# Performance work log

Hardware: AMD Instinct MI355X
Metric: run time of the kernel (lower is better)

The kernel has to match this reference:

```python
import jax, jax.numpy as jnp
import numpy as np

# dims: T tokens, HID hidden, H heads, D head_dim, K conv kernel size
T, HID, H, D, K = 4096, 2048, 16, 128, 4
HD = H * D
EPS = 1e-6


def causal_conv(x, w):
    # depthwise causal conv: x [T, C], w [C, K]; y_t = sum_i w[:, i] * x_{t-K+1+i}
    xp = jnp.pad(x, ((K - 1, 0), (0, 0)))
    y = jnp.zeros_like(x)
    for i in range(K):  # small fixed kernel loop
        y = y + w[:, i] * xp[i:i + x.shape[0]]
    return y


def l2norm(x):
    return x * jax.lax.rsqrt(jnp.sum(x * x, -1, keepdims=True) + EPS)


def setup_inputs() -> dict:
    key = jax.random.key(0)
    ks = jax.random.split(key, 16)
    s = lambda n: 1.0 / np.sqrt(n)
    return {
        "hidden_states": jax.random.normal(ks[0], (T, HID), jnp.float32),
        "Wq": jax.random.normal(ks[1], (HID, HD), jnp.float32) * s(HID),
        "Wk": jax.random.normal(ks[2], (HID, HD), jnp.float32) * s(HID),
        "Wv": jax.random.normal(ks[3], (HID, HD), jnp.float32) * s(HID),
        "wq_conv": jax.random.normal(ks[4], (HD, K), jnp.float32) * s(K),
        "wk_conv": jax.random.normal(ks[5], (HD, K), jnp.float32) * s(K),
        "wv_conv": jax.random.normal(ks[6], (HD, K), jnp.float32) * s(K),
        "A_log": jax.random.uniform(ks[7], (H,), jnp.float32, 0.0, 0.5),
        "dt_bias": jax.random.normal(ks[8], (HD,), jnp.float32) * 0.1,
        "Wfa": jax.random.normal(ks[9], (HID, D), jnp.float32) * s(HID),
        "Wfb": jax.random.normal(ks[10], (D, HD), jnp.float32) * s(D),
        "Wb": jax.random.normal(ks[11], (HID, H), jnp.float32) * s(HID),
        "Wga": jax.random.normal(ks[12], (HID, D), jnp.float32) * s(HID),
        "Wgb": jax.random.normal(ks[13], (D, HD), jnp.float32) * s(D),
        "norm_w": jnp.ones((D,), jnp.float32),
        "Wo": jax.random.normal(ks[14], (HD, HID), jnp.float32) * s(HD),
    }


def reference(hidden_states, Wq, Wk, Wv, wq_conv, wk_conv, wv_conv, A_log,
              dt_bias, Wfa, Wfb, Wb, Wga, Wgb, norm_w, Wo):
    x = hidden_states
    # projections + short causal conv + SiLU
    q = jax.nn.silu(causal_conv(x @ Wq, wq_conv)).reshape(T, H, D)
    k = jax.nn.silu(causal_conv(x @ Wk, wk_conv)).reshape(T, H, D)
    v = jax.nn.silu(causal_conv(x @ Wv, wv_conv)).reshape(T, H, D)
    # fine-grained per-channel log-decay: g = -exp(A_log) * softplus(f + dt_bias), [T,H,D]
    f = (x @ Wfa) @ Wfb + dt_bias
    g = -(jnp.exp(A_log)[None, :, None]) * jax.nn.softplus(f.reshape(T, H, D))
    beta = jax.nn.sigmoid(x @ Wb)  # [T, H]
    q = l2norm(q)
    k = l2norm(k)
    scale = D ** -0.5

    def step(S, inp):  # S: [H, Dk, Dv]
        q_t, k_t, v_t, g_t, b_t = inp
        S = S * jnp.exp(g_t)[..., None]  # diagonal per-key-channel decay
        err = v_t - jnp.einsum('hkv,hk->hv', S, k_t)  # delta-rule error
        dv = b_t[:, None] * err  # beta gate
        S = S + k_t[:, :, None] * dv[:, None, :]
        o_t = jnp.einsum('hkv,hk->hv', S, q_t) * scale
        return S, o_t

    S0 = jnp.zeros((H, D, D), jnp.float32)
    _, o = jax.lax.scan(step, S0, (q, k, v, g, beta))  # o: [T, H, D]

    # gated RMSNorm then output projection
    gate = ((x @ Wga) @ Wgb).reshape(T, H, D)
    o = o * jax.lax.rsqrt(jnp.mean(o * o, -1, keepdims=True) + EPS)
    o = o * norm_w * jax.nn.silu(gate)
    return o.reshape(T, HD) @ Wo
```

## Files before the change

### kernel.cpp

```cpp
#include <hip/hip_runtime.h>
#include <hip/hip_bf16.h>
#include <math.h>

typedef __bf16 bf16_t;
typedef __bf16 bf16x8 __attribute__((ext_vector_type(8)));
typedef float  floatx4 __attribute__((ext_vector_type(4)));
typedef float  floatx2 __attribute__((ext_vector_type(2)));
typedef unsigned uintx4 __attribute__((ext_vector_type(4)));

constexpr int T_TOK = 4096;
constexpr int HID   = 2048;
constexpr int NH    = 16;
constexpr int DH    = 128;
constexpr int CH    = 2048;
constexpr int CHUNK = 16;
constexpr int NCH   = T_TOK / CHUNK;

__global__ __launch_bounds__(256) void cast_to_bf16(const float* __restrict__ in,
                                                    bf16_t* __restrict__ out, int n) {
  int i = (blockIdx.x * 256 + threadIdx.x) * 8;
  if (i >= n) return;
  float4 a = *(const float4*)(in + i);
  float4 b = *(const float4*)(in + i + 4);
  bf16x8 o;
  o[0]=(bf16_t)a.x; o[1]=(bf16_t)a.y; o[2]=(bf16_t)a.z; o[3]=(bf16_t)a.w;
  o[4]=(bf16_t)b.x; o[5]=(bf16_t)b.y; o[6]=(bf16_t)b.z; o[7]=(bf16_t)b.w;
  *(bf16x8*)(out + i) = o;
}

__global__ __launch_bounds__(256) void transpose_cast(const float* __restrict__ in,
                                                      bf16_t* __restrict__ out, int R, int C) {
  __shared__ float tile[32][33];
  int tx = threadIdx.x & 31;
  int ty = threadIdx.x >> 5;
  int r0 = blockIdx.x * 32;
  int c0 = blockIdx.y * 32;
#pragma unroll
  for (int i = 0; i < 4; i++) {
    int r = ty + i * 8;
    float v = 0.f;
    if (r0 + r < R && c0 + tx < C) v = in[(size_t)(r0 + r) * C + (c0 + tx)];
    tile[r][tx] = v;
  }
  __syncthreads();
#pragma unroll
  for (int i = 0; i < 4; i++) {
    int cr = ty + i * 8;
    if (c0 + cr < C && r0 + tx < R)
      out[(size_t)(c0 + cr) * R + (r0 + tx)] = (bf16_t)tile[tx][cr];
  }
}

template<bool OUT_BF16>
__global__ __launch_bounds__(256) void gemm_bf16(
    const bf16_t* __restrict__ A, int lda,
    const bf16_t* __restrict__ Bt, int ldb,
    void* __restrict__ Cv, int ldc, int M, int N, int K) {
  __shared__ bf16_t sA[128][40];
  __shared__ bf16_t sB[128][40];
  const int tid  = threadIdx.x;
  const int bm0  = blockIdx.x * 128;
  const int bn0  = blockIdx.y * 128;
  const int wave = tid >> 6;
  const int lane = tid & 63;
  const int wm   = (wave & 1) * 64;
  const int wn   = (wave >> 1) * 64;
  const int fm   = lane & 15;
  const int kq   = lane >> 4;

  floatx4 acc[4][4];
#pragma unroll
  for (int mi = 0; mi < 4; mi++)
#pragma unroll
    for (int ni = 0; ni < 4; ni++)
      acc[mi][ni] = (floatx4){0.f, 0.f, 0.f, 0.f};

  const int sr = tid >> 2;
  const int sk = (tid & 3) * 8;
  const bool bval0 = (bn0 + sr) < N;
  const bool bval1 = (bn0 + sr + 64) < N;
  const bf16_t* Ag0 = A + (size_t)(bm0 + sr) * lda + sk;
  const bf16_t* Ag1 = Ag0 + (size_t)64 * lda;
  const bf16_t* Bg0 = Bt + (size_t)(bn0 + sr) * ldb + sk;
  const bf16_t* Bg1 = Bg0 + (size_t)64 * ldb;

  for (int k0 = 0; k0 < K; k0 += 32) {
    float4 a0 = *(const float4*)(Ag0 + k0);
    float4 a1 = *(const float4*)(Ag1 + k0);
    float4 b0 = bval0 ? *(const float4*)(Bg0 + k0) : make_float4(0.f, 0.f, 0.f, 0.f);
    float4 b1 = bval1 ? *(const float4*)(Bg1 + k0) : make_float4(0.f, 0.f, 0.f, 0.f);
    __syncthreads();
    *(float4*)(&sA[sr][sk])      = a0;
    *(float4*)(&sA[sr + 64][sk]) = a1;
    *(float4*)(&sB[sr][sk])      = b0;
    *(float4*)(&sB[sr + 64][sk]) = b1;
    __syncthreads();
    bf16x8 afr[4], bfr[4];
#pragma unroll
    for (int i = 0; i < 4; i++) {
      afr[i] = *(const bf16x8*)(&sA[wm + i * 16 + fm][kq * 8]);
      bfr[i] = *(const bf16x8*)(&sB[wn + i * 16 + fm][kq * 8]);
    }
#pragma unroll
    for (int mi = 0; mi < 4; mi++)
#pragma unroll
      for (int ni = 0; ni < 4; ni++)
        acc[mi][ni] = __builtin_amdgcn_mfma_f32_16x16x32_bf16(afr[mi], bfr[ni], acc[mi][ni], 0, 0, 0);
  }

  const int rr = (lane >> 4) * 4;
#pragma unroll
  for (int mi = 0; mi < 4; mi++) {
#pragma unroll
    for (int r = 0; r < 4; r++) {
      const int row = bm0 + wm + mi * 16 + rr + r;
#pragma unroll
      for (int ni = 0; ni < 4; ni++) {
        const int col = bn0 + wn + ni * 16 + fm;
        if (col < N) {
          if constexpr (OUT_BF16)
            ((bf16_t*)Cv)[(size_t)row * ldc + col] = (bf16_t)acc[mi][ni][r];
          else
            ((float*)Cv)[(size_t)row * ldc + col] = acc[mi][ni][r];
        }
      }
    }
  }
}

template<bool L2NORM>
__global__ __launch_bounds__(256) void conv_silu(
    const bf16_t* __restrict__ raw, const float* __restrict__ wconv,
    bf16_t* __restrict__ out) {
  const int t   = blockIdx.x;
  const int tid = threadIdx.x;
  const int c0  = tid * 8;

  float w[8][4];
#pragma unroll
  for (int j = 0; j < 8; j++) {
    float4 t0 = *(const float4*)(wconv + (size_t)(c0 + j) * 4);
    w[j][0] = t0.x; w[j][1] = t0.y; w[j][2] = t0.z; w[j][3] = t0.w;
  }
  float a[8] = {};
#pragma unroll
  for (int i = 0; i < 4; i++) {
    int tr = t - 3 + i;
    if (tr < 0) continue;
    bf16x8 xr = *(const bf16x8*)(raw + (size_t)tr * CH + c0);
#pragma unroll
    for (int j = 0; j < 8; j++) a[j] += w[j][i] * (float)xr[j];
  }
  float s = 0.f;
#pragma unroll
  for (int j = 0; j < 8; j++) {
    a[j] = a[j] / (1.f + expf(-a[j]));
    s += a[j] * a[j];
  }
  float rs = 1.f;
  if constexpr (L2NORM) {
#pragma unroll
    for (int m = 1; m < 16; m <<= 1) s += __shfl_xor(s, m);
    rs = rsqrtf(s + 1e-6f);
  }
  bf16x8 r;
#pragma unroll
  for (int j = 0; j < 8; j++) r[j] = (bf16_t)(a[j] * rs);
  *(bf16x8*)(out + (size_t)t * CH + c0) = r;
}

__global__ __launch_bounds__(256) void gamma_beta(
    float* __restrict__ f_gam, const float* __restrict__ dt_bias,
    const float* __restrict__ A_log, float* __restrict__ beta_io) {
  const int t   = blockIdx.x;
  const int tid = threadIdx.x;
  const int c0  = tid * 8;
  const int h   = c0 >> 7;
  const float a_h = expf(A_log[h]);
  const size_t o0 = (size_t)t * CH + c0;
  float fv[8], db[8];
  { float4 f0 = *(const float4*)(f_gam + o0);   float4 f1 = *(const float4*)(f_gam + o0 + 4);
    fv[0]=f0.x; fv[1]=f0.y; fv[2]=f0.z; fv[3]=f0.w; fv[4]=f1.x; fv[5]=f1.y; fv[6]=f1.z; fv[7]=f1.w;
    float4 d0 = *(const float4*)(dt_bias + c0); float4 d1 = *(const float4*)(dt_bias + c0 + 4);
    db[0]=d0.x; db[1]=d0.y; db[2]=d0.z; db[3]=d0.w; db[4]=d1.x; db[5]=d1.y; db[6]=d1.z; db[7]=d1.w; }
  float og[8];
#pragma unroll
  for (int j = 0; j < 8; j++) {
    float f = fv[j] + db[j];
    float sp = (f > 20.f) ? f : log1pf(expf(f));
    og[j] = -a_h * sp;
  }
  *(float4*)(f_gam + o0)     = make_float4(og[0], og[1], og[2], og[3]);
  *(float4*)(f_gam + o0 + 4) = make_float4(og[4], og[5], og[6], og[7]);
  if (tid < NH) {
    float b = beta_io[(size_t)t * NH + tid];
    beta_io[(size_t)t * NH + tid] = 1.f / (1.f + expf(-b));
  }
}

template<int IMM>
__device__ __forceinline__ float swzf(float x) {
  return __builtin_bit_cast(float, __builtin_amdgcn_ds_swizzle(__builtin_bit_cast(int, x), IMM));
}
template<int CTRL>
__device__ __forceinline__ float dppadd(float x) {
  int v = __builtin_amdgcn_update_dpp(0, __builtin_bit_cast(int, x), CTRL, 0xF, 0xF, true);
  return x + __builtin_bit_cast(float, v);
}
__device__ __forceinline__ float cumsum16(float x) {
  x = dppadd<0x111>(x);
  x = dppadd<0x112>(x);
  x = dppadd<0x114>(x);
  x = dppadd<0x118>(x);
  return x;
}
__device__ __forceinline__ float bperm(int lane, float x) {
  return __builtin_bit_cast(float, __builtin_amdgcn_ds_bpermute(lane << 2, __builtin_bit_cast(int, x)));
}
__device__ __forceinline__ floatx2 bfpair(unsigned u) {
  floatx2 r;
  r[0] = __builtin_bit_cast(float, u << 16);
  r[1] = __builtin_bit_cast(float, u & 0xFFFF0000u);
  return r;
}

__global__ __launch_bounds__(64) void wy_prep(
    bf16_t* __restrict__ qn, bf16_t* __restrict__ kn,
    const float* __restrict__ gg, const float* __restrict__ beta,
    bf16_t* __restrict__ ktilT, float* __restrict__ Tm,
    bf16_t* __restrict__ MBf, float* __restrict__ ecT, float* __restrict__ e2T) {
  const int hc = blockIdx.x;
  const int h  = hc >> 8;
  const int c  = hc & 255;
  const int l  = threadIdx.x;
  const int tl = l & 15;
  const int gr = l >> 4;

  __shared__ bf16_t KldsT[128][24];
  __shared__ float  Wlds[16][17];
  __shared__ float  Mlds[16][17];
  __shared__ float  eclds[128], e2lds[128];
  __shared__ float  blds[16];

  const int kb0 = h * DH + gr * 8;
  const size_t rowoff = (size_t)(c * CHUNK + tl) * CH;

  if (gr == 0) blds[tl] = beta[(size_t)(c * CHUNK + tl) * NH + h];

  floatx4 wt = (floatx4){0.f, 0.f, 0.f, 0.f};
  floatx4 m  = (floatx4){0.f, 0.f, 0.f, 0.f};
  bf16x8 khs[4], qhs[4];
#pragma unroll
  for (int kb = 0; kb < 4; kb++) {
    const int ke = kb0 + kb * 32;
    float4 ga = *(const float4*)(gg + rowoff + ke);
    float4 gb = *(const float4*)(gg + rowoff + ke + 4);
    float cm[8] = {ga.x, ga.y, ga.z, ga.w, gb.x, gb.y, gb.z, gb.w};
    float lamh[8], lamt[8], ec[8], e2[8];
#pragma unroll
    for (int j = 0; j < 8; j++) {
      float cs   = cumsum16(cm[j]);
      float cmid = swzf<(7 << 5) | 0x10>(cs);
      lamh[j] = __expf(cs - cmid);
      lamt[j] = __expf(cmid - cs);
      ec[j]   = __expf(cmid);
      e2[j]   = swzf<(15 << 5) | 0x10>(lamh[j]);
    }
    if (tl == 0) {
#pragma unroll
      for (int j = 0; j < 8; j++) {
        eclds[kb * 32 + gr * 8 + j] = ec[j];
        e2lds[kb * 32 + gr * 8 + j] = e2[j];
      }
    }
    uint4 kr = *(const uint4*)(kn + rowoff + ke);
    uint4 qr = *(const uint4*)(qn + rowoff + ke);
    float kf[8], qf[8];
    { floatx2 a0 = bfpair(kr.x), a1 = bfpair(kr.y), a2 = bfpair(kr.z), a3 = bfpair(kr.w);
      kf[0]=a0[0];kf[1]=a0[1];kf[2]=a1[0];kf[3]=a1[1];kf[4]=a2[0];kf[5]=a2[1];kf[6]=a3[0];kf[7]=a3[1];
      floatx2 b0 = bfpair(qr.x), b1 = bfpair(qr.y), b2 = bfpair(qr.z), b3 = bfpair(qr.w);
      qf[0]=b0[0];qf[1]=b0[1];qf[2]=b1[0];qf[3]=b1[1];qf[4]=b2[0];qf[5]=b2[1];qf[6]=b3[0];qf[7]=b3[1]; }
    bf16x8 khat, ktil, qhat;
#pragma unroll
    for (int j = 0; j < 8; j++) {
      khat[j] = (bf16_t)(kf[j] * lamh[j]);
      ktil[j] = (bf16_t)(kf[j] * lamt[j]);
      qhat[j] = (bf16_t)(qf[j] * lamh[j]);
      khs[kb][j] = (bf16_t)(kf[j] * lamh[j] * ec[j]);
      qhs[kb][j] = (bf16_t)(qf[j] * lamh[j] * ec[j]);
    }
    wt = __builtin_amdgcn_mfma_f32_16x16x32_bf16(ktil, khat, wt, 0, 0, 0);
    m  = __builtin_amdgcn_mfma_f32_16x16x32_bf16(qhat, ktil, m,  0, 0, 0);
#pragma unroll
    for (int j = 0; j < 8; j++) KldsT[kb * 32 + gr * 8 + j][tl] = ktil[j];
  }
#pragma unroll
  for (int kb = 0; kb < 4; kb++) {
    *(uint4*)(kn + rowoff + kb0 + kb * 32) = __builtin_bit_cast(uint4, khs[kb]);
    *(uint4*)(qn + rowoff + kb0 + kb * 32) = __builtin_bit_cast(uint4, qhs[kb]);
  }
#pragma unroll
  for (int ri = 0; ri < 4; ri++) {
    Wlds[tl][4 * gr + ri] = wt[ri];
    Mlds[4 * gr + ri][tl] = (4 * gr + ri >= tl) ? m[ri] : 0.f;
  }
  {
    const int j = tl;
    float x[16];
#pragma unroll
    for (int t = 0; t < 16; t++) {
      float a = 0.f;
#pragma unroll
      for (int s = 0; s < 16; s++)
        if (s < t) a = fmaf(Wlds[t][s], x[s], a);
      x[t] = (t == j) ? 1.f : ((t > j) ? -blds[t] * a : 0.f);
    }
    if (gr == 0) {
      const float bj = blds[j];
#pragma unroll
      for (int t = 0; t < 16; t++)
        Tm[((size_t)hc * 16 + t) * 16 + j] = x[t] * bj;
    }
  }
  {
    uint4 mbo = {0, 0, 0, 0};
    if (gr < 2) {
      bf16x8 mm;
#pragma unroll
      for (int jj = 0; jj < 8; jj++) mm[jj] = (bf16_t)Mlds[tl][gr * 8 + jj];
      mbo = __builtin_bit_cast(uint4, mm);
    }
    ((uint4*)MBf)[(size_t)hc * 64 + l] = mbo;
  }
  for (int i = l; i < 128; i += 64) {
    uint4 a0 = *(const uint4*)&KldsT[i][0];
    uint4 a1 = *(const uint4*)&KldsT[i][8];
    bf16_t* dst = ktilT + ((size_t)hc * 128 + i) * 16;
    *(uint4*)dst = a0;
    *(uint4*)(dst + 8) = a1;
  }
  for (int i = l; i < 128; i += 64) {
    ecT[(size_t)hc * 128 + (i & 15) * 8 + (i >> 4)] = eclds[i];
    e2T[(size_t)hc * 128 + (i & 15) * 8 + (i >> 4)] = e2lds[i];
  }
}

__global__ __launch_bounds__(128, 1) void scan_wy3(
    const bf16_t* __restrict__ khsG, const bf16_t* __restrict__ qhsG,
    const bf16_t* __restrict__ vn, const bf16_t* __restrict__ ktilT,
    const float* __restrict__ Tm, const bf16_t* __restrict__ MBf,
    const float* __restrict__ ecT, const float* __restrict__ e2T,
    float* __restrict__ o) {
  const int h   = blockIdx.x >> 3;
  const int vt  = blockIdx.x & 7;
  const int tid = threadIdx.x;
  const int wid = tid >> 6;
  const int l   = tid & 63;
  const int tl  = l & 15;
  const int gr  = l >> 4;

  __shared__ uint4   sKQ[2][8][64];
  __shared__ floatx4 sT[2][4][64];
  __shared__ uint4   sMB[2][64];
  __shared__ uint4   sKT[2][8][64];
  __shared__ floatx4 sEC[2][4][64];
  __shared__ uint2   sV[2][64];
  __shared__ float   SldsT[16][132];
  __shared__ float   DVlds[16][17];

  const int kb0 = h * DH + gr * 8;
  const int vb0 = h * DH + vt * 16 + gr * 4;
  const size_t hcBase = (size_t)h * NCH;
  constexpr float scale = 0.08838834764831845f;

  auto produce = [&](int c, int b) {
    const size_t rowoff = (size_t)(c * CHUNK + tl) * CH;
    const size_t hc = hcBase + c;
    uint4 kq[8];
#pragma unroll
    for (int kb = 0; kb < 4; kb++) {
      kq[kb]     = *(const uint4*)(khsG + rowoff + kb0 + kb * 32);
      kq[4 + kb] = *(const uint4*)(qhsG + rowoff + kb0 + kb * 32);
    }
    const float* Trp = Tm + (hc * 16 + tl) * 16;
    floatx4 Tv[4];
#pragma unroll
    for (int j = 0; j < 4; j++) Tv[j] = *(const floatx4*)(Trp + 4 * j);
    uint4 mbv = ((const uint4*)MBf)[hc * 64 + l];
    const int g2 = gr & 1;
    uint4 ktv[8];
#pragma unroll
    for (int kt = 0; kt < 8; kt++)
      ktv[kt] = *(const uint4*)(ktilT + (hc * 128 + kt * 16 + tl) * 16 + g2 * 8);
    floatx4 ecv[4];
    ecv[0] = *(const floatx4*)(ecT + hc * 128 + tl * 8);
    ecv[1] = *(const floatx4*)(ecT + hc * 128 + tl * 8 + 4);
    ecv[2] = *(const floatx4*)(e2T + hc * 128 + tl * 8);
    ecv[3] = *(const floatx4*)(e2T + hc * 128 + tl * 8 + 4);
    uint2 vv = *(const uint2*)(vn + rowoff + vb0);
#pragma unroll
    for (int i = 0; i < 8; i++) sKQ[b][i][l] = kq[i];
#pragma unroll
    for (int j = 0; j < 4; j++) sT[b][j][l] = Tv[j];
    sMB[b][l] = mbv;
#pragma unroll
    for (int i = 0; i < 8; i++) sKT[b][i][l] = ktv[i];
#pragma unroll
    for (int j = 0; j < 4; j++) sEC[b][j][l] = ecv[j];
    sV[b][l] = vv;
  };

  float S[8][4];
#pragma unroll
  for (int kt = 0; kt < 8; kt++)
#pragma unroll
    for (int ri = 0; ri < 4; ri++) S[kt][ri] = 0.f;

  if (wid == 1) {
    produce(0, 0);
  } else {
    for (int i = l; i < 16 * 132; i += 64) (&SldsT[0][0])[i] = 0.f;
  }
  __syncthreads();

  int cur = 0;
  for (int c = 0; c < NCH; ++c) {
    if (wid == 1) {
      produce(c + 1 < NCH ? c + 1 : NCH - 1, cur ^ 1);
    } else {
      const size_t rowoff = (size_t)(c * CHUNK + tl) * CH;
      floatx4 p  = (floatx4){0.f, 0.f, 0.f, 0.f};
      floatx4 o1 = (floatx4){0.f, 0.f, 0.f, 0.f};
#pragma unroll
      for (int kb = 0; kb < 4; kb++) {
        float4 sa = *(const float4*)(&SldsT[tl][kb * 32 + gr * 8]);
        float4 sb = *(const float4*)(&SldsT[tl][kb * 32 + gr * 8 + 4]);
        bf16x8 s0a;
        s0a[0]=(bf16_t)sa.x; s0a[1]=(bf16_t)sa.y; s0a[2]=(bf16_t)sa.z; s0a[3]=(bf16_t)sa.w;
        s0a[4]=(bf16_t)sb.x; s0a[5]=(bf16_t)sb.y; s0a[6]=(bf16_t)sb.z; s0a[7]=(bf16_t)sb.w;
        p  = __builtin_amdgcn_mfma_f32_16x16x32_bf16(s0a, __builtin_bit_cast(bf16x8, sKQ[cur][kb][l]), p,  0, 0, 0);
        o1 = __builtin_amdgcn_mfma_f32_16x16x32_bf16(s0a, __builtin_bit_cast(bf16x8, sKQ[cur][4 + kb][l]), o1, 0, 0, 0);
      }
      float acc[4];
      { uint2 vr = sV[cur][l];
        floatx2 v01 = bfpair(vr.x), v23 = bfpair(vr.y);
        acc[0] = v01[0] - p[0]; acc[1] = v01[1] - p[1];
        acc[2] = v23[0] - p[2]; acc[3] = v23[1] - p[3]; }
      floatx4 T0 = sT[cur][0][l], T1 = sT[cur][1][l], T2 = sT[cur][2][l], T3 = sT[cur][3][l];
      float dv[4] = {0.f, 0.f, 0.f, 0.f};
#pragma unroll
      for (int s = 0; s < 16; s++) {
        const float ts = (s < 4) ? T0[s] : (s < 8) ? T1[s - 4] : (s < 12) ? T2[s - 8] : T3[s - 12];
#pragma unroll
        for (int ri = 0; ri < 4; ri++)
          dv[ri] = fmaf(ts, bperm((gr << 4) | s, acc[ri]), dv[ri]);
      }
#pragma unroll
      for (int ri = 0; ri < 4; ri++) DVlds[tl][4 * gr + ri] = dv[ri];
      bf16x8 dva = {};
      if (gr < 2) {
#pragma unroll
        for (int jj = 0; jj < 8; jj++) dva[jj] = (bf16_t)DVlds[gr * 8 + jj][tl];
      }
      floatx4 o2 = __builtin_amdgcn_mfma_f32_16x16x32_bf16(
          dva, __builtin_bit_cast(bf16x8, sMB[cur][l]), (floatx4){0.f, 0.f, 0.f, 0.f}, 0, 0, 0);
      { float4 ov = make_float4((o1[0] + o2[0]) * scale, (o1[1] + o2[1]) * scale,
                                (o1[2] + o2[2]) * scale, (o1[3] + o2[3]) * scale);
        *(float4*)(o + rowoff + vb0) = ov; }
      floatx4 ec0 = sEC[cur][0][l], ec1 = sEC[cur][1][l];
      floatx4 e20 = sEC[cur][2][l], e21 = sEC[cur][3][l];
#pragma unroll
      for (int kt = 0; kt < 8; kt++) {
        const float ecK = (kt < 4) ? ec0[kt] : ec1[kt - 4];
        const float e2K = (kt < 4) ? e20[kt] : e21[kt - 4];
        floatx4 sa;
#pragma unroll
        for (int ri = 0; ri < 4; ri++) sa[ri] = ecK * S[kt][ri];
        sa = __builtin_amdgcn_mfma_f32_16x16x32_bf16(
            dva, __builtin_bit_cast(bf16x8, sKT[cur][kt][l]), sa, 0, 0, 0);
#pragma unroll
        for (int ri = 0; ri < 4; ri++) S[kt][ri] = e2K * sa[ri];
      }
#pragma unroll
      for (int kt = 0; kt < 8; kt++)
#pragma unroll
        for (int ri = 0; ri < 4; ri++)
          SldsT[4 * gr + ri][kt * 16 + tl] = S[kt][ri];
    }
    __syncthreads();
    cur ^= 1;
  }
}

__global__ __launch_bounds__(256) void postprocess(
    const float* __restrict__ o, const bf16_t* __restrict__ gate,
    const float* __restrict__ norm_w, bf16_t* __restrict__ og) {
  const int t = blockIdx.x, tid = threadIdx.x;
  const int c0 = tid * 8, d0 = c0 & 127;
  const size_t o0 = (size_t)t * CH + c0;
  float ov[8], gv[8], nw[8];
  { float4 a = *(const float4*)(o + o0);    float4 b = *(const float4*)(o + o0 + 4);
    ov[0]=a.x; ov[1]=a.y; ov[2]=a.z; ov[3]=a.w; ov[4]=b.x; ov[5]=b.y; ov[6]=b.z; ov[7]=b.w;
    bf16x8 g8 = *(const bf16x8*)(gate + o0);
    for (int j = 0; j < 8; j++) gv[j] = (float)g8[j];
    float4 e = *(const float4*)(norm_w + d0); float4 f = *(const float4*)(norm_w + d0 + 4);
    nw[0]=e.x; nw[1]=e.y; nw[2]=e.z; nw[3]=e.w; nw[4]=f.x; nw[5]=f.y; nw[6]=f.z; nw[7]=f.w; }
  float ss = 0.f;
#pragma unroll
  for (int j = 0; j < 8; j++) ss += ov[j] * ov[j];
#pragma unroll
  for (int m = 1; m < 16; m <<= 1) ss += __shfl_xor(ss, m);
  const float rs = rsqrtf(ss * (1.f / 128.f) + 1e-6f);
  bf16x8 r;
#pragma unroll
  for (int j = 0; j < 8; j++) {
    float g = gv[j];
    float val = ov[j] * rs * nw[j] * (g / (1.f + expf(-g)));
    r[j] = (bf16_t)val;
  }
  *(bf16x8*)(og + o0) = r;
}

static inline void launch_gemm(const bf16_t* A, int lda, const bf16_t* Bt, int ldb,
                               void* C, int ldc, int M, int N, int K, bool obf16,
                               hipStream_t s) {
  dim3 grid(M / 128, (N + 127) / 128);
  if (obf16) gemm_bf16<true><<<grid, 256, 0, s>>>(A, lda, Bt, ldb, C, ldc, M, N, K);
  else       gemm_bf16<false><<<grid, 256, 0, s>>>(A, lda, Bt, ldb, C, ldc, M, N, K);
}

extern "C" void kernel_launch(void* const* d_in, const int* in_sizes, int n_in,
                              void* d_out, int out_size, void* d_ws, size_t ws_size,
                              hipStream_t stream) {
  const float* x       = (const float*)d_in[0];
  const float* Wq      = (const float*)d_in[1];
  const float* Wk      = (const float*)d_in[2];
  const float* Wv      = (const float*)d_in[3];
  const float* wqc     = (const float*)d_in[4];
  const float* wkc     = (const float*)d_in[5];
  const float* wvc     = (const float*)d_in[6];
  const float* A_log   = (const float*)d_in[7];
  const float* dt_bias = (const float*)d_in[8];
  const float* Wfa     = (const float*)d_in[9];
  const float* Wfb     = (const float*)d_in[10];
  const float* Wb      = (const float*)d_in[11];
  const float* Wga     = (const float*)d_in[12];
  const float* Wgb     = (const float*)d_in[13];
  const float* norm_w  = (const float*)d_in[14];
  const float* Wo      = (const float*)d_in[15];

  char* w = (char*)d_ws;
  size_t off = 0;
  auto give = [&](size_t bytes) -> void* {
    size_t cur = off;
    off = (off + bytes + 255) & ~(size_t)255;
    return (void*)(w + cur);
  };
  bf16_t* Wbig = (bf16_t*)give((size_t)CH * HID * 2);
  bf16_t* WfaT = (bf16_t*)give((size_t)128 * HID * 2);
  bf16_t* WgaT = (bf16_t*)give((size_t)128 * HID * 2);
  bf16_t* WfbT = (bf16_t*)give((size_t)CH * 128 * 2);
  bf16_t* WgbT = (bf16_t*)give((size_t)CH * 128 * 2);
  bf16_t* WbT  = (bf16_t*)give((size_t)NH * HID * 2);
  bf16_t* Ax   = (bf16_t*)give((size_t)T_TOK * HID * 2);
  bf16_t* raw0 = (bf16_t*)give((size_t)T_TOK * CH * 2);
  bf16_t* qnb  = (bf16_t*)give((size_t)T_TOK * CH * 2);
  bf16_t* knb  = (bf16_t*)give((size_t)T_TOK * CH * 2);
  bf16_t* vnb  = (bf16_t*)give((size_t)T_TOK * CH * 2);
  bf16_t* f1b  = (bf16_t*)give((size_t)T_TOK * 128 * 2);
  bf16_t* g1b  = (bf16_t*)give((size_t)T_TOK * 128 * 2);
  float*  fbuf = (float*)give((size_t)T_TOK * CH * 4);
  bf16_t* gateb= (bf16_t*)give((size_t)T_TOK * CH * 2);
  float*  betab= (float*)give((size_t)T_TOK * NH * 4);
  bf16_t* ktilT= (bf16_t*)give((size_t)NH * NCH * 128 * 16 * 2);
  float*  Tmat = (float*)give((size_t)NH * NCH * 256 * 4);
  bf16_t* MBf  = (bf16_t*)give((size_t)NH * NCH * 64 * 8 * 2);
  float*  ecTb = (float*)give((size_t)NH * NCH * 128 * 4);
  float*  e2Tb = (float*)give((size_t)NH * NCH * 128 * 4);
  float*  obuf = (float*)Ax;
  bf16_t* ogb  = qnb;

  auto tr = [&](const float* in, bf16_t* out, int R, int C) {
    transpose_cast<<<dim3((R + 31) / 32, (C + 31) / 32), 256, 0, stream>>>(in, out, R, C);
  };

  cast_to_bf16<<<dim3((T_TOK * HID) / 2048), 256, 0, stream>>>(x, Ax, T_TOK * HID);
  tr(Wfa, WfaT, HID, 128); tr(Wga, WgaT, HID, 128);
  tr(Wfb, WfbT, 128, CH);  tr(Wgb, WgbT, 128, CH);
  tr(Wb, WbT, HID, NH);

  tr(Wq, Wbig, HID, CH);
  launch_gemm(Ax, HID, Wbig, HID, raw0, CH, T_TOK, CH, HID, true, stream);
  conv_silu<true><<<dim3(T_TOK), 256, 0, stream>>>(raw0, wqc, qnb);
  tr(Wk, Wbig, HID, CH);
  launch_gemm(Ax, HID, Wbig, HID, raw0, CH, T_TOK, CH, HID, true, stream);
  conv_silu<true><<<dim3(T_TOK), 256, 0, stream>>>(raw0, wkc, knb);
  tr(Wv, Wbig, HID, CH);
  launch_gemm(Ax, HID, Wbig, HID, raw0, CH, T_TOK, CH, HID, true, stream);
  conv_silu<false><<<dim3(T_TOK), 256, 0, stream>>>(raw0, wvc, vnb);

  launch_gemm(Ax, HID, WfaT, HID, f1b, 128, T_TOK, 128, HID, true, stream);
  launch_gemm(Ax, HID, WgaT, HID, g1b, 128, T_TOK, 128, HID, true, stream);
  launch_gemm(Ax, HID, WbT, HID, betab, NH, T_TOK, NH, HID, false, stream);
  launch_gemm(f1b, 128, WfbT, 128, fbuf, CH, T_TOK, CH, 128, false, stream);
  launch_gemm(g1b, 128, WgbT, 128, gateb, CH, T_TOK, CH, 128, true, stream);
  gamma_beta<<<dim3(T_TOK), 256, 0, stream>>>(fbuf, dt_bias, A_log, betab);

  wy_prep<<<dim3(NH * NCH), 64, 0, stream>>>(qnb, knb, fbuf, betab,
                                             ktilT, Tmat, MBf, ecTb, e2Tb);
  scan_wy3<<<dim3(128), 128, 0, stream>>>(knb, qnb, vnb, ktilT, Tmat, MBf,
                                          ecTb, e2Tb, obuf);

  postprocess<<<dim3(T_TOK), 256, 0, stream>>>(obuf, gateb, norm_w, ogb);

  tr(Wo, Wbig, CH, HID);
  launch_gemm(ogb, CH, Wbig, CH, (float*)d_out, HID, T_TOK, HID, CH, false, stream);
}
```

Baseline: 1.070 ms.

## Add direct global-to-LDS GEMM path and replace bperm exchange with LDS reads

Adds a GEMM variant that uses global_load_lds to move A/B tiles straight into shared memory without passing through registers. It is selected whenever N is a multiple of 128. In the recurrence kernel, the cross-lane bperm shuffles of the delta-rule error are replaced by a float4 LDS store followed by vectorized LDS reads. The new GEMM is single-buffered with two barriers per k-step, so there is no load/compute overlap, and the LDS tile layout may cause bank conflicts.

```diff
diff --git a/kernel.cpp b/kernel.cpp
--- a/kernel.cpp
+++ b/kernel.cpp
@@ -128,6 +128,85 @@
   }
 }
 
+__device__ __forceinline__ void gload_lds16(const bf16_t* g, bf16_t* l) {
+  __builtin_amdgcn_global_load_lds(
+      (const __attribute__((address_space(1))) void*)g,
+      (__attribute__((address_space(3))) void*)l, 16, 0, 0);
+}
+
+template<bool OUT_BF16>
+__global__ __launch_bounds__(256) void gemm_bf16_lds(
+    const bf16_t* __restrict__ A, int lda,
+    const bf16_t* __restrict__ Bt, int ldb,
+    void* __restrict__ Cv, int ldc, int M, int N, int K) {
+  __shared__ bf16_t sA[128][32];
+  __shared__ bf16_t sB[128][32];
+  const int tid  = threadIdx.x;
+  const int bm0  = blockIdx.x * 128;
+  const int bn0  = blockIdx.y * 128;
+  const int wave = tid >> 6;
+  const int lane = tid & 63;
+  const int wm   = (wave & 1) * 64;
+  const int wn   = (wave >> 1) * 64;
+  const int fm   = lane & 15;
+  const int kq   = lane >> 4;
+
+  floatx4 acc[4][4];
+#pragma unroll
+  for (int mi = 0; mi < 4; mi++)
+#pragma unroll
+    for (int ni = 0; ni < 4; ni++)
+      acc[mi][ni] = (floatx4){0.f, 0.f, 0.f, 0.f};
+
+  const int sr = tid >> 2;
+  const int sk = (tid & 3) * 8;
+  const bf16_t* Ag0 = A + (size_t)(bm0 + sr) * lda + sk;
+  const bf16_t* Ag1 = Ag0 + (size_t)64 * lda;
+  const bf16_t* Bg0 = Bt + (size_t)(bn0 + sr) * ldb + sk;
+  const bf16_t* Bg1 = Bg0 + (size_t)64 * ldb;
+  bf16_t* ldsA0 = &sA[16 * wave][0];
+  bf16_t* ldsA1 = &sA[64 + 16 * wave][0];
+  bf16_t* ldsB0 = &sB[16 * wave][0];
+  bf16_t* ldsB1 = &sB[64 + 16 * wave][0];
+
+  for (int k0 = 0; k0 < K; k0 += 32) {
+    __syncthreads();
+    gload_lds16(Ag0 + k0, ldsA0);
+    gload_lds16(Ag1 + k0, ldsA1);
+    gload_lds16(Bg0 + k0, ldsB0);
+    gload_lds16(Bg1 + k0, ldsB1);
+    __syncthreads();
+    bf16x8 afr[4], bfr[4];
+#pragma unroll
+    for (int i = 0; i < 4; i++) {
+      afr[i] = *(const bf16x8*)(&sA[wm + i * 16 + fm][kq * 8]);
+      bfr[i] = *(const bf16x8*)(&sB[wn + i * 16 + fm][kq * 8]);
+    }
+#pragma unroll
+    for (int mi = 0; mi < 4; mi++)
+#pragma unroll
+      for (int ni = 0; ni < 4; ni++)
+        acc[mi][ni] = __builtin_amdgcn_mfma_f32_16x16x32_bf16(afr[mi], bfr[ni], acc[mi][ni], 0, 0, 0);
+  }
+
+  const int rr = (lane >> 4) * 4;
+#pragma unroll
+  for (int mi = 0; mi < 4; mi++) {
+#pragma unroll
+    for (int r = 0; r < 4; r++) {
+      const int row = bm0 + wm + mi * 16 + rr + r;
+#pragma unroll
+      for (int ni = 0; ni < 4; ni++) {
+        const int col = bn0 + wn + ni * 16 + fm;
+        if constexpr (OUT_BF16)
+          ((bf16_t*)Cv)[(size_t)row * ldc + col] = (bf16_t)acc[mi][ni][r];
+        else
+          ((float*)Cv)[(size_t)row * ldc + col] = acc[mi][ni][r];
+      }
+    }
+  }
+}
+
 template<bool L2NORM>
 __global__ __launch_bounds__(256) void conv_silu(
     const bf16_t* __restrict__ raw, const float* __restrict__ wconv,
@@ -446,14 +525,17 @@
         floatx2 v01 = bfpair(vr.x), v23 = bfpair(vr.y);
         acc[0] = v01[0] - p[0]; acc[1] = v01[1] - p[1];
         acc[2] = v23[0] - p[2]; acc[3] = v23[1] - p[3]; }
+      *(float4*)(&DVlds[tl][4 * gr]) = make_float4(acc[0], acc[1], acc[2], acc[3]);
       floatx4 T0 = sT[cur][0][l], T1 = sT[cur][1][l], T2 = sT[cur][2][l], T3 = sT[cur][3][l];
       float dv[4] = {0.f, 0.f, 0.f, 0.f};
 #pragma unroll
       for (int s = 0; s < 16; s++) {
         const float ts = (s < 4) ? T0[s] : (s < 8) ? T1[s - 4] : (s < 12) ? T2[s - 8] : T3[s - 12];
-#pragma unroll
-        for (int ri = 0; ri < 4; ri++)
-          dv[ri] = fmaf(ts, bperm((gr << 4) | s, acc[ri]), dv[ri]);
+        float4 vp = *(const float4*)(&DVlds[s][4 * gr]);
+        dv[0] = fmaf(ts, vp.x, dv[0]);
+        dv[1] = fmaf(ts, vp.y, dv[1]);
+        dv[2] = fmaf(ts, vp.z, dv[2]);
+        dv[3] = fmaf(ts, vp.w, dv[3]);
       }
 #pragma unroll
       for (int ri = 0; ri < 4; ri++) DVlds[tl][4 * gr + ri] = dv[ri];
@@ -525,8 +607,13 @@
                                void* C, int ldc, int M, int N, int K, bool obf16,
                                hipStream_t s) {
   dim3 grid(M / 128, (N + 127) / 128);
-  if (obf16) gemm_bf16<true><<<grid, 256, 0, s>>>(A, lda, Bt, ldb, C, ldc, M, N, K);
-  else       gemm_bf16<false><<<grid, 256, 0, s>>>(A, lda, Bt, ldb, C, ldc, M, N, K);
+  if ((N & 127) == 0) {
+    if (obf16) gemm_bf16_lds<true><<<grid, 256, 0, s>>>(A, lda, Bt, ldb, C, ldc, M, N, K);
+    else       gemm_bf16_lds<false><<<grid, 256, 0, s>>>(A, lda, Bt, ldb, C, ldc, M, N, K);
+  } else {
+    if (obf16) gemm_bf16<true><<<grid, 256, 0, s>>>(A, lda, Bt, ldb, C, ldc, M, N, K);
+    else       gemm_bf16<false><<<grid, 256, 0, s>>>(A, lda, Bt, ldb, C, ldc, M, N, K);
+  }
 }
 
 extern "C" void kernel_launch(void* const* d_in, const int* in_sizes, int n_in,
```

After: 1.025 ms. -4.2%, faster.
